# Optimization experiments

Measured on AMD Instinct MI355X. Metric: run time of the kernel, lower is better.

The kernel has to match this reference:

```python
import jax, jax.numpy as jnp
import numpy as np

B, L, S, D, H, E, UV = 4, 2048, 2048, 1024, 8, 128, 128
ROT_DIM = H * E  # RotaryEmbedding(dim=qk_size*n_heads) applied on flattened dim


def gelu(x):
    return jax.nn.gelu(x, approximate=False)  # torch nn.GELU default (erf)


def rope(x):
    # x: [B, T, ROT_DIM]; interleaved-pair rotary (lucidrains rotary_embedding_torch default)
    T = x.shape[1]
    inv_freq = 1.0 / (10000.0 ** (jnp.arange(0, ROT_DIM, 2, dtype=jnp.float32) / ROT_DIM))
    freqs = jnp.arange(T, dtype=jnp.float32)[:, None] * inv_freq  # [T, ROT_DIM/2]
    cos = jnp.repeat(jnp.cos(freqs), 2, axis=-1)  # [T, ROT_DIM]
    sin = jnp.repeat(jnp.sin(freqs), 2, axis=-1)
    xp = x.reshape(*x.shape[:-1], ROT_DIM // 2, 2)
    x_rot = jnp.stack([-xp[..., 1], xp[..., 0]], axis=-1).reshape(x.shape)
    return x * cos + x_rot * sin


def setup_inputs() -> dict:
    key = jax.random.key(0)
    ks = jax.random.split(key, 16)
    n = lambda k, sh, s=1.0: jax.random.normal(k, sh, jnp.float32) * s
    w = 0.02
    return {
        "u": n(ks[0], (B, L, D)),
        "queries": n(ks[1], (B, L, D)),
        "keys": n(ks[2], (B, S, D)),
        "values": n(ks[3], (B, S, D)),
        "Wqk": n(ks[4], (D, H * E), w), "bqk": jnp.zeros((H * E,), jnp.float32),
        "Wv": n(ks[5], (D, H * UV), w), "bv": jnp.zeros((H * UV,), jnp.float32),
        "Wu": n(ks[6], (D, H * UV), w), "bu": jnp.zeros((H * UV,), jnp.float32),
        "Wo": n(ks[7], (H * UV, D), w), "bo": jnp.zeros((D,), jnp.float32),
        "q_gamma": jnp.ones((E,), jnp.float32), "q_beta": n(ks[8], (E,), w),
        "k_gamma": jnp.ones((E,), jnp.float32), "k_beta": n(ks[9], (E,), w),
    }


def _forward(u, queries, keys, values, Wqk, bqk, Wv, bv, Wu, bu, Wo, bo,
             q_gamma, q_beta, k_gamma, k_beta):
    # use_aff=True: shared qk projection + per-branch ScaleOffset over qk_size
    qk = gelu(queries @ Wqk + bqk)                      # [B,L,H*E]
    qk4 = qk.reshape(B, L, H, E)
    q = (qk4 * q_gamma + q_beta).reshape(B, L, H * E)
    k = (qk4 * k_gamma + k_beta).reshape(B, L, H * E)
    q = rope(q).reshape(B, L, H, E)
    k = rope(k).reshape(B, S, H, E)
    v = gelu(values @ Wv + bv).reshape(B, S, H, UV)
    # Conv1d(kernel_size=1) == pointwise linear over channels
    u_p = gelu(u @ Wu + bu).reshape(B, L, H, UV)
    scale = 1.0 / jnp.sqrt(jnp.float32(E))
    scores = jnp.einsum("blhe,bshe->bhls", q, k) * scale
    attn = jax.nn.softmax(scores, axis=-1)              # [B,H,L,S]
    ctx = jnp.einsum("bhls,bshd->blhd", attn, v)        # [B,L,H,UV]
    out = (u_p * ctx).reshape(B, L, H * UV)             # gate by u
    o = out @ Wo + bo                                   # [B,L,D]
    return o, attn


def reference(u, queries, keys, values, Wqk, bqk, Wv, bv, Wu, bu, Wo, bo,
              q_gamma, q_beta, k_gamma, k_beta):
    return _forward(u, queries, keys, values, Wqk, bqk, Wv, bv, Wu, bu, Wo, bo,
                    q_gamma, q_beta, k_gamma, k_beta)
```

## Files before the change

kernel.cpp:

```cpp
#include <hip/hip_runtime.h>
#include <hip/hip_bf16.h>
#include <math.h>

#define DEVI static __device__ __forceinline__

typedef __attribute__((ext_vector_type(4))) float f32x4;
typedef __attribute__((ext_vector_type(8))) short bf16x8;
typedef __attribute__((ext_vector_type(4))) short bf16x4;

constexpr int Bc = 4, Lc = 2048, Sc = 2048, Dc = 1024, Hc = 8, Ec = 128, UVc = 128;
constexpr int HEc = Hc * Ec;
constexpr int BLc = Bc * Lc;

DEVI unsigned f2bf_bits(float f) {
  unsigned u = __builtin_bit_cast(unsigned, f);
  return (u + 0x7FFFu + ((u >> 16) & 1u)) >> 16;
}
DEVI short f2bf(float f) { return (short)f2bf_bits(f); }
DEVI float bf2f(short s) {
  return __builtin_bit_cast(float, (unsigned)((unsigned short)s) << 16);
}
DEVI float gelu_f(float x) { return 0.5f * x * (1.0f + erff(x * 0.7071067811865476f)); }

DEVI void gload16(const void* gsrc, void* ldst) {
  __builtin_amdgcn_global_load_lds(
      (const __attribute__((address_space(1))) unsigned*)gsrc,
      (__attribute__((address_space(3))) unsigned*)(ldst), 16, 0, 0);
}

DEVI f32x4 mfma16(bf16x8 a, bf16x8 b, f32x4 c) {
  return __builtin_amdgcn_mfma_f32_16x16x32_bf16(a, b, c, 0, 0, 0);
}

__global__ void cvt_bf16_kernel(const float* __restrict__ in, short* __restrict__ out) {
  size_t i = ((size_t)blockIdx.x * 256 + threadIdx.x) * 8;
  float4 f1 = *reinterpret_cast<const float4*>(in + i);
  float4 f2 = *reinterpret_cast<const float4*>(in + i + 4);
  uint4 pk;
  pk.x = f2bf_bits(f1.x) | (f2bf_bits(f1.y) << 16);
  pk.y = f2bf_bits(f1.z) | (f2bf_bits(f1.w) << 16);
  pk.z = f2bf_bits(f2.x) | (f2bf_bits(f2.y) << 16);
  pk.w = f2bf_bits(f2.z) | (f2bf_bits(f2.w) << 16);
  *reinterpret_cast<uint4*>(out + i) = pk;
}

__global__ void wt_trans_kernel(const float* __restrict__ W, short* __restrict__ WT) {
  __shared__ float t[32][33];
  int tx = threadIdx.x, ty = threadIdx.y;
  int n0 = blockIdx.x * 32, k0 = blockIdx.y * 32;
#pragma unroll
  for (int i = 0; i < 4; i++) {
    int r = ty + i * 8;
    t[r][tx] = W[(size_t)(k0 + r) * 1024 + n0 + tx];
  }
  __syncthreads();
#pragma unroll
  for (int i = 0; i < 4; i++) {
    int r = ty + i * 8;
    WT[(size_t)(n0 + r) * 1024 + k0 + tx] = f2bf(t[tx][r]);
  }
}

__global__ void rope_table_kernel(float* __restrict__ ct, float* __restrict__ st) {
  int idx = blockIdx.x * 256 + threadIdx.x;
  int t = idx >> 9, i = idx & 511;
  float inv = expf((float)i * (-9.210340371976184f / 512.0f));
  float ang = (float)t * inv;
  float sv, cv;
  sincosf(ang, &sv, &cv);
  ct[idx] = cv;
  st[idx] = sv;
}

template <bool GELU_OUT>
__global__ __launch_bounds__(256, 2) void gemm_kernel(
    const short* __restrict__ A, const short* __restrict__ BT,
    const float* __restrict__ bias, void* __restrict__ Cptr, int M, int N, int K) {
  __shared__ char smem[32768];
  const int tid = threadIdx.x;
  const int wave = tid >> 6, lane = tid & 63;
  const int lquad = lane >> 4, l15 = lane & 15;
  const int m0 = blockIdx.x * 128, n0 = blockIdx.y * 128;
  const int wr = wave >> 1, wc = wave & 1;
  f32x4 acc[4][4] = {};

  const int q0 = tid * 16, q1 = tid * 16 + 4096;
  const int r0 = q0 >> 6, o0 = (q0 & 63) ^ ((r0 & 3) << 4);
  const int r1 = q1 >> 6, o1 = (q1 & 63) ^ ((r1 & 3) << 4);
  const short* a0 = A + (size_t)(m0 + r0) * K + (o0 >> 1);
  const short* a1 = A + (size_t)(m0 + r1) * K + (o1 >> 1);
  const short* b0 = BT + (size_t)(n0 + r0) * K + (o0 >> 1);
  const short* b1 = BT + (size_t)(n0 + r1) * K + (o1 >> 1);

#define G_STAGE(buf, kt)                                   \
  {                                                        \
    char* As_ = smem + (buf)*8192;                         \
    char* Bs_ = smem + 16384 + (buf)*8192;                 \
    gload16(a0 + (kt), As_ + q0);                          \
    gload16(a1 + (kt), As_ + q1);                          \
    gload16(b0 + (kt), Bs_ + q0);                          \
    gload16(b1 + (kt), Bs_ + q1);                          \
  }

  G_STAGE(0, 0);
  asm volatile("s_waitcnt vmcnt(0)" ::: "memory");
  __builtin_amdgcn_s_barrier();

  const int NT = K >> 5;
  for (int t = 0; t < NT; t++) {
    const int cur = t & 1;
    if (t + 1 < NT) G_STAGE(cur ^ 1, (t + 1) * 32);
    __builtin_amdgcn_sched_barrier(0);
    const char* As_ = smem + cur * 8192;
    const char* Bs_ = smem + 16384 + cur * 8192;
    const int ko = lquad * 16;
    bf16x8 a[4], b[4];
#pragma unroll
    for (int f = 0; f < 4; f++) {
      int ra = wr * 64 + f * 16 + l15;
      a[f] = *reinterpret_cast<const bf16x8*>(As_ + ra * 64 + (ko ^ ((ra & 3) << 4)));
      int rb = wc * 64 + f * 16 + l15;
      b[f] = *reinterpret_cast<const bf16x8*>(Bs_ + rb * 64 + (ko ^ ((rb & 3) << 4)));
    }
#pragma unroll
    for (int mf = 0; mf < 4; mf++)
#pragma unroll
      for (int nf = 0; nf < 4; nf++)
        acc[mf][nf] = mfma16(a[mf], b[nf], acc[mf][nf]);
    asm volatile("s_waitcnt vmcnt(0) lgkmcnt(0)" ::: "memory");
    __builtin_amdgcn_sched_barrier(0);
    __builtin_amdgcn_s_barrier();
  }
#undef G_STAGE

#pragma unroll
  for (int mf = 0; mf < 4; mf++) {
#pragma unroll
    for (int nf = 0; nf < 4; nf++) {
      int mrow = m0 + wr * 64 + mf * 16 + 4 * lquad;
      int ncol = n0 + wc * 64 + nf * 16 + l15;
      float bval = bias[ncol];
#pragma unroll
      for (int r = 0; r < 4; r++) {
        float v = acc[mf][nf][r] + bval;
        if (GELU_OUT) {
          ((short*)Cptr)[(size_t)(mrow + r) * N + ncol] = f2bf(gelu_f(v));
        } else {
          ((float*)Cptr)[(size_t)(mrow + r) * N + ncol] = v;
        }
      }
    }
  }
}

__global__ void rope_apply_kernel(const short* __restrict__ qkg,
                                  const float* __restrict__ ct, const float* __restrict__ st,
                                  const float* __restrict__ qg, const float* __restrict__ qb,
                                  const float* __restrict__ kg, const float* __restrict__ kb,
                                  short* __restrict__ qo, short* __restrict__ ko) {
  int tid = blockIdx.x * 256 + threadIdx.x;
  size_t base = (size_t)tid * 8;
  int bl = (int)(base >> 10);
  int rem = (int)(base & 1023);
  int e0 = rem & 127;
  int t = bl & 2047;
  int pf = rem >> 1;
  uint4 raw = *reinterpret_cast<const uint4*>(qkg + base);
  short sh[8];
  *reinterpret_cast<uint4*>(sh) = raw;
  float4 c4 = *reinterpret_cast<const float4*>(ct + (size_t)t * 512 + pf);
  float4 s4 = *reinterpret_cast<const float4*>(st + (size_t)t * 512 + pf);
  float4 qga = *reinterpret_cast<const float4*>(qg + e0);
  float4 qgb = *reinterpret_cast<const float4*>(qg + e0 + 4);
  float4 qba = *reinterpret_cast<const float4*>(qb + e0);
  float4 qbb = *reinterpret_cast<const float4*>(qb + e0 + 4);
  float4 kga = *reinterpret_cast<const float4*>(kg + e0);
  float4 kgb = *reinterpret_cast<const float4*>(kg + e0 + 4);
  float4 kba = *reinterpret_cast<const float4*>(kb + e0);
  float4 kbb = *reinterpret_cast<const float4*>(kb + e0 + 4);
  float C[4] = {c4.x, c4.y, c4.z, c4.w};
  float Sn[4] = {s4.x, s4.y, s4.z, s4.w};
  float QG[8] = {qga.x, qga.y, qga.z, qga.w, qgb.x, qgb.y, qgb.z, qgb.w};
  float QB[8] = {qba.x, qba.y, qba.z, qba.w, qbb.x, qbb.y, qbb.z, qbb.w};
  float KG[8] = {kga.x, kga.y, kga.z, kga.w, kgb.x, kgb.y, kgb.z, kgb.w};
  float KB[8] = {kba.x, kba.y, kba.z, kba.w, kbb.x, kbb.y, kbb.z, kbb.w};
  short qsh[8], ksh[8];
#pragma unroll
  for (int j = 0; j < 4; j++) {
    float x0 = bf2f(sh[2 * j]), x1 = bf2f(sh[2 * j + 1]);
    float q0 = x0 * QG[2 * j] + QB[2 * j];
    float q1 = x1 * QG[2 * j + 1] + QB[2 * j + 1];
    qsh[2 * j] = f2bf(q0 * C[j] - q1 * Sn[j]);
    qsh[2 * j + 1] = f2bf(q1 * C[j] + q0 * Sn[j]);
    float k0v = x0 * KG[2 * j] + KB[2 * j];
    float k1v = x1 * KG[2 * j + 1] + KB[2 * j + 1];
    ksh[2 * j] = f2bf(k0v * C[j] - k1v * Sn[j]);
    ksh[2 * j + 1] = f2bf(k1v * C[j] + k0v * Sn[j]);
  }
  *reinterpret_cast<uint4*>(qo + base) = *reinterpret_cast<uint4*>(qsh);
  *reinterpret_cast<uint4*>(ko + base) = *reinterpret_cast<uint4*>(ksh);
}

__global__ void vtrans_kernel(const short* __restrict__ v, short* __restrict__ vT) {
  __shared__ short t[32][33];
  int bh = blockIdx.z;
  int b = bh >> 3, h = bh & 7;
  int s0 = blockIdx.x * 32, d0 = blockIdx.y * 32;
  int tx = threadIdx.x, ty = threadIdx.y;
#pragma unroll
  for (int i = 0; i < 4; i++) {
    int s = ty + i * 8;
    t[s][tx] = v[(((size_t)b * Sc + s0 + s) * Hc + h) * UVc + d0 + tx];
  }
  __syncthreads();
#pragma unroll
  for (int i = 0; i < 4; i++) {
    int d = ty + i * 8;
    vT[((size_t)bh * UVc + d0 + d) * Sc + s0 + tx] = t[tx][d];
  }
}

__global__ __launch_bounds__(256, 2) void attn_kernel(
    const short* __restrict__ qs, const short* __restrict__ ks,
    const short* __restrict__ vT, const short* __restrict__ up,
    float* __restrict__ attn_out, short* __restrict__ gate) {
  __shared__ char smem[65536];
  const int bid = blockIdx.x;
  const int xcd = bid & 7, jj = bid >> 3;
  const int bh = xcd * 4 + (jj >> 4);
  const int lblk = jj & 15;
  const int b = bh >> 3, h = bh & 7;
  const int l0 = lblk * 128;
  const int tid = threadIdx.x;
  const int wave = tid >> 6, lane = tid & 63;
  const int lquad = lane >> 4, l15 = lane & 15;
  const float scale = 0.08838834764831845f;

  const short* ksrc[4];
  const short* vsrc[4];
  int qdst[4];
#pragma unroll
  for (int i = 0; i < 4; i++) {
    int q = i * 4096 + tid * 16;
    qdst[i] = q;
    int row = q >> 8, off = (q & 255) ^ ((row & 7) << 4);
    ksrc[i] = ks + (((size_t)b * Sc + row) * Hc + h) * Ec + (off >> 1);
    int rv = q >> 7, ov = (q & 127) ^ ((rv & 7) << 4);
    vsrc[i] = vT + ((size_t)bh * UVc + rv) * Sc + (ov >> 1);
  }

#define STAGE_K(buf, s0)                                                     \
  {                                                                          \
    char* Kb_ = smem + (buf)*16384;                                          \
    gload16(ksrc[0] + (size_t)(s0)*1024, Kb_ + qdst[0]);                     \
    gload16(ksrc[1] + (size_t)(s0)*1024, Kb_ + qdst[1]);                     \
    gload16(ksrc[2] + (size_t)(s0)*1024, Kb_ + qdst[2]);                     \
    gload16(ksrc[3] + (size_t)(s0)*1024, Kb_ + qdst[3]);                     \
  }
#define STAGE_V(buf, s0)                                                     \
  {                                                                          \
    char* Vb_ = smem + 32768 + (buf)*16384;                                  \
    gload16(vsrc[0] + (s0), Vb_ + qdst[0]);                                  \
    gload16(vsrc[1] + (s0), Vb_ + qdst[1]);                                  \
    gload16(vsrc[2] + (s0), Vb_ + qdst[2]);                                  \
    gload16(vsrc[3] + (s0), Vb_ + qdst[3]);                                  \
  }

  bf16x8 qf[2][4];
#pragma unroll
  for (int cf = 0; cf < 2; cf++) {
    int lrow = l0 + wave * 32 + cf * 16 + l15;
    const short* qp = qs + (((size_t)b * Lc + lrow) * Hc + h) * Ec;
#pragma unroll
    for (int kt = 0; kt < 4; kt++)
      qf[cf][kt] = *reinterpret_cast<const bf16x8*>(qp + kt * 32 + lquad * 8);
  }

#define QK_TILE(KBASE, d)                                                              \
  {                                                                                    \
    const char* KB_ = (KBASE);                                                         \
    _Pragma("unroll") for (int kt = 0; kt < 4; kt++) {                                 \
      _Pragma("unroll") for (int sf = 0; sf < 4; sf++) {                               \
        int row = sf * 16 + l15;                                                       \
        bf16x8 kf = *reinterpret_cast<const bf16x8*>(                                  \
            KB_ + row * 256 + ((kt * 64 + lquad * 16) ^ ((row & 7) << 4)));            \
        d[sf][0] = mfma16(kf, qf[0][kt], d[sf][0]);                                    \
        d[sf][1] = mfma16(kf, qf[1][kt], d[sf][1]);                                    \
      }                                                                                \
    }                                                                                  \
  }

  STAGE_K(0, 0);
  asm volatile("s_waitcnt vmcnt(0)" ::: "memory");
  __builtin_amdgcn_s_barrier();
  float rs0 = 0.f, rs1 = 0.f;
  for (int t = 0; t < 32; t++) {
    const int cur = t & 1;
    if (t < 31) STAGE_K(cur ^ 1, (t + 1) * 64);
    __builtin_amdgcn_sched_barrier(0);
    f32x4 d[4][2] = {};
    QK_TILE(smem + cur * 16384, d);
#pragma unroll
    for (int sf = 0; sf < 4; sf++)
#pragma unroll
      for (int r = 0; r < 4; r++) {
        rs0 += __expf(scale * d[sf][0][r]);
        rs1 += __expf(scale * d[sf][1][r]);
      }
    asm volatile("s_waitcnt vmcnt(0) lgkmcnt(0)" ::: "memory");
    __builtin_amdgcn_sched_barrier(0);
    __builtin_amdgcn_s_barrier();
  }
  rs0 += __shfl_xor(rs0, 16);
  rs0 += __shfl_xor(rs0, 32);
  rs1 += __shfl_xor(rs1, 16);
  rs1 += __shfl_xor(rs1, 32);
  const float rcp0 = 1.0f / rs0, rcp1 = 1.0f / rs1;

  STAGE_K(0, 0);
  STAGE_V(0, 0);
  asm volatile("s_waitcnt vmcnt(0)" ::: "memory");
  __builtin_amdgcn_s_barrier();
  f32x4 ctx[8][2] = {};
  for (int t = 0; t < 32; t++) {
    const int cur = t & 1;
    const int s0 = t * 64;
    if (t < 31) {
      STAGE_K(cur ^ 1, s0 + 64);
      STAGE_V(cur ^ 1, s0 + 64);
    }
    __builtin_amdgcn_sched_barrier(0);
    f32x4 d[4][2] = {};
    QK_TILE(smem + cur * 16384, d);
#pragma unroll
    for (int sf = 0; sf < 4; sf++)
#pragma unroll
      for (int r = 0; r < 4; r++) {
        d[sf][0][r] = __expf(scale * d[sf][0][r]) * rcp0;
        d[sf][1][r] = __expf(scale * d[sf][1][r]) * rcp1;
      }
#pragma unroll
    for (int cf = 0; cf < 2; cf++) {
      int lrow = l0 + wave * 32 + cf * 16 + l15;
      float* arow = attn_out + ((size_t)bh * Lc + lrow) * Sc + s0 + lquad * 4;
#pragma unroll
      for (int sf = 0; sf < 4; sf++)
        *reinterpret_cast<f32x4*>(arow + sf * 16) = d[sf][cf];
    }
    const char* VB_ = smem + 32768 + cur * 16384;
#pragma unroll
    for (int c = 0; c < 2; c++) {
      bf16x8 pb0, pb1;
#pragma unroll
      for (int r = 0; r < 4; r++) {
        pb0[r] = f2bf(d[2 * c][0][r]);
        pb0[4 + r] = f2bf(d[2 * c + 1][0][r]);
        pb1[r] = f2bf(d[2 * c][1][r]);
        pb1[4 + r] = f2bf(d[2 * c + 1][1][r]);
      }
#pragma unroll
      for (int df = 0; df < 8; df++) {
        int dd = df * 16 + l15;
        int sw = (dd & 7) << 4;
        const char* vrow = VB_ + dd * 128;
        bf16x4 lo = *reinterpret_cast<const bf16x4*>(vrow + ((c * 64 + lquad * 8) ^ sw));
        bf16x4 hi = *reinterpret_cast<const bf16x4*>(vrow + ((c * 64 + 32 + lquad * 8) ^ sw));
        bf16x8 vf = __builtin_shufflevector(lo, hi, 0, 1, 2, 3, 4, 5, 6, 7);
        ctx[df][0] = mfma16(vf, pb0, ctx[df][0]);
        ctx[df][1] = mfma16(vf, pb1, ctx[df][1]);
      }
    }
    asm volatile("s_waitcnt vmcnt(8) lgkmcnt(0)" ::: "memory");
    __builtin_amdgcn_sched_barrier(0);
    __builtin_amdgcn_s_barrier();
  }
#undef STAGE_K
#undef STAGE_V
#undef QK_TILE

#pragma unroll
  for (int cf = 0; cf < 2; cf++) {
    int lrow = l0 + wave * 32 + cf * 16 + l15;
    size_t base = ((size_t)b * Lc + lrow) * HEc + h * UVc;
    const short* ub = up + base;
    short* gp = gate + base;
#pragma unroll
    for (int df = 0; df < 8; df++) {
      int doff = df * 16 + lquad * 4;
      bf16x4 uv = *reinterpret_cast<const bf16x4*>(ub + doff);
      bf16x4 gv;
#pragma unroll
      for (int r = 0; r < 4; r++)
        gv[r] = f2bf(bf2f(uv[r]) * ctx[df][cf][r]);
      *reinterpret_cast<bf16x4*>(gp + doff) = gv;
    }
  }
}

extern "C" void kernel_launch(void* const* d_in, const int* in_sizes, int n_in,
                              void* d_out, int out_size, void* d_ws, size_t ws_size,
                              hipStream_t stream) {
  const float* u_in = (const float*)d_in[0];
  const float* qry = (const float*)d_in[1];
  const float* vals = (const float*)d_in[3];
  const float* Wqk = (const float*)d_in[4];
  const float* bqk = (const float*)d_in[5];
  const float* Wv = (const float*)d_in[6];
  const float* bv = (const float*)d_in[7];
  const float* Wu = (const float*)d_in[8];
  const float* bu = (const float*)d_in[9];
  const float* Wo = (const float*)d_in[10];
  const float* bo = (const float*)d_in[11];
  const float* qg = (const float*)d_in[12];
  const float* qb = (const float*)d_in[13];
  const float* kg = (const float*)d_in[14];
  const float* kb = (const float*)d_in[15];

  char* w = (char*)d_ws;
  short* WT0 = (short*)w; w += (size_t)1024 * 1024 * 2;
  short* WT1 = (short*)w; w += (size_t)1024 * 1024 * 2;
  short* WT2 = (short*)w; w += (size_t)1024 * 1024 * 2;
  short* WT3 = (short*)w; w += (size_t)1024 * 1024 * 2;
  float* ctab = (float*)w; w += (size_t)2048 * 512 * 4;
  float* stab = (float*)w; w += (size_t)2048 * 512 * 4;
  const size_t BUF = (size_t)BLc * HEc * 2;
  short* C1 = (short*)w; w += BUF;
  short* C2 = (short*)w; w += BUF;
  short* C3 = (short*)w; w += BUF;
  short* qkg = (short*)w; w += BUF;
  short* qbf = (short*)w; w += BUF;
  short* kbf = (short*)w; w += BUF;
  short* vTb = (short*)w; w += BUF;
  short* upb = (short*)w; w += BUF;
  short* vgl = C1;
  short* gtb = qkg;

  float* o_out = (float*)d_out;
  float* attn_out = o_out + (size_t)BLc * Dc;

  dim3 tb(32, 8);
  cvt_bf16_kernel<<<4096, 256, 0, stream>>>(qry, C1);
  cvt_bf16_kernel<<<4096, 256, 0, stream>>>(vals, C2);
  cvt_bf16_kernel<<<4096, 256, 0, stream>>>(u_in, C3);
  wt_trans_kernel<<<dim3(32, 32), tb, 0, stream>>>(Wqk, WT0);
  wt_trans_kernel<<<dim3(32, 32), tb, 0, stream>>>(Wv, WT1);
  wt_trans_kernel<<<dim3(32, 32), tb, 0, stream>>>(Wu, WT2);
  wt_trans_kernel<<<dim3(32, 32), tb, 0, stream>>>(Wo, WT3);
  rope_table_kernel<<<4096, 256, 0, stream>>>(ctab, stab);

  gemm_kernel<true><<<dim3(64, 8), 256, 0, stream>>>(C1, WT0, bqk, qkg, BLc, HEc, Dc);
  rope_apply_kernel<<<4096, 256, 0, stream>>>(qkg, ctab, stab, qg, qb, kg, kb, qbf, kbf);
  gemm_kernel<true><<<dim3(64, 8), 256, 0, stream>>>(C2, WT1, bv, vgl, BLc, HEc, Dc);
  vtrans_kernel<<<dim3(64, 4, 32), tb, 0, stream>>>(vgl, vTb);
  gemm_kernel<true><<<dim3(64, 8), 256, 0, stream>>>(C3, WT2, bu, upb, BLc, HEc, Dc);
  attn_kernel<<<512, 256, 0, stream>>>(qbf, kbf, vTb, upb, attn_out, gtb);
  gemm_kernel<false><<<dim3(64, 8), 256, 0, stream>>>(gtb, WT3, bo, o_out, BLc, Dc, HEc);
}
```

Baseline: 422.4 us.

## Fuse fp32 conversion and rope into GEMMs, deepen K pipeline, stream attn stores

Drops the separate fp32→bf16 conversion kernels: the GEMM now loads fp32 activations into registers and converts them while writing to LDS. The rope/scale-offset step is fused into the QK GEMM epilogue, using a combined cos/sin table and a lane shuffle to fetch the pair partner. The four weight transposes are merged into one launch. The attention kernel's first pass gets a 4-deep K prefetch ring with partial vmcnt waits, and attention probability stores become nontemporal. Together these cut intermediate HBM traffic and launches, at the cost of register-path A loads in the GEMM and more scattered epilogue stores.

```diff
diff --git a/kernel.cpp b/kernel.cpp
--- a/kernel.cpp
+++ b/kernel.cpp
@@ -32,20 +32,15 @@
   return __builtin_amdgcn_mfma_f32_16x16x32_bf16(a, b, c, 0, 0, 0);
 }
 
-__global__ void cvt_bf16_kernel(const float* __restrict__ in, short* __restrict__ out) {
-  size_t i = ((size_t)blockIdx.x * 256 + threadIdx.x) * 8;
-  float4 f1 = *reinterpret_cast<const float4*>(in + i);
-  float4 f2 = *reinterpret_cast<const float4*>(in + i + 4);
-  uint4 pk;
-  pk.x = f2bf_bits(f1.x) | (f2bf_bits(f1.y) << 16);
-  pk.y = f2bf_bits(f1.z) | (f2bf_bits(f1.w) << 16);
-  pk.z = f2bf_bits(f2.x) | (f2bf_bits(f2.y) << 16);
-  pk.w = f2bf_bits(f2.z) | (f2bf_bits(f2.w) << 16);
-  *reinterpret_cast<uint4*>(out + i) = pk;
-}
-
-__global__ void wt_trans_kernel(const float* __restrict__ W, short* __restrict__ WT) {
+__global__ void wt_trans_kernel(const float* __restrict__ W0, const float* __restrict__ W1,
+                                const float* __restrict__ W2, const float* __restrict__ W3,
+                                short* __restrict__ T0, short* __restrict__ T1,
+                                short* __restrict__ T2, short* __restrict__ T3) {
   __shared__ float t[32][33];
+  const float* Ws[4] = {W0, W1, W2, W3};
+  short* Ts[4] = {T0, T1, T2, T3};
+  const float* W = Ws[blockIdx.z];
+  short* WT = Ts[blockIdx.z];
   int tx = threadIdx.x, ty = threadIdx.y;
   int n0 = blockIdx.x * 32, k0 = blockIdx.y * 32;
 #pragma unroll
@@ -61,21 +56,23 @@
   }
 }
 
-__global__ void rope_table_kernel(float* __restrict__ ct, float* __restrict__ st) {
+__global__ void rope_cs_kernel(float2* __restrict__ cs) {
   int idx = blockIdx.x * 256 + threadIdx.x;
   int t = idx >> 9, i = idx & 511;
   float inv = expf((float)i * (-9.210340371976184f / 512.0f));
-  float ang = (float)t * inv;
   float sv, cv;
-  sincosf(ang, &sv, &cv);
-  ct[idx] = cv;
-  st[idx] = sv;
-}
-
-template <bool GELU_OUT>
+  sincosf((float)t * inv, &sv, &cv);
+  cs[idx] = make_float2(cv, sv);
+}
+
+template <bool AF32, int EPI>
 __global__ __launch_bounds__(256, 2) void gemm_kernel(
-    const short* __restrict__ A, const short* __restrict__ BT,
-    const float* __restrict__ bias, void* __restrict__ Cptr, int M, int N, int K) {
+    const void* __restrict__ Aptr, const short* __restrict__ BT,
+    const float* __restrict__ bias, void* __restrict__ Cptr,
+    const float2* __restrict__ cstab,
+    const float* __restrict__ qg, const float* __restrict__ qb,
+    const float* __restrict__ kg, const float* __restrict__ kb,
+    short* __restrict__ qout, short* __restrict__ kout, int M, int N, int K) {
   __shared__ char smem[32768];
   const int tid = threadIdx.x;
   const int wave = tid >> 6, lane = tid & 63;
@@ -87,29 +84,78 @@
   const int q0 = tid * 16, q1 = tid * 16 + 4096;
   const int r0 = q0 >> 6, o0 = (q0 & 63) ^ ((r0 & 3) << 4);
   const int r1 = q1 >> 6, o1 = (q1 & 63) ^ ((r1 & 3) << 4);
-  const short* a0 = A + (size_t)(m0 + r0) * K + (o0 >> 1);
-  const short* a1 = A + (size_t)(m0 + r1) * K + (o1 >> 1);
   const short* b0 = BT + (size_t)(n0 + r0) * K + (o0 >> 1);
   const short* b1 = BT + (size_t)(n0 + r1) * K + (o1 >> 1);
-
-#define G_STAGE(buf, kt)                                   \
-  {                                                        \
-    char* As_ = smem + (buf)*8192;                         \
-    char* Bs_ = smem + 16384 + (buf)*8192;                 \
-    gload16(a0 + (kt), As_ + q0);                          \
-    gload16(a1 + (kt), As_ + q1);                          \
-    gload16(b0 + (kt), Bs_ + q0);                          \
-    gload16(b1 + (kt), Bs_ + q1);                          \
-  }
-
-  G_STAGE(0, 0);
-  asm volatile("s_waitcnt vmcnt(0)" ::: "memory");
+  const short* a0 = nullptr;
+  const short* a1 = nullptr;
+  const float* asrc = nullptr;
+  int arow = 0, ao0 = 0, ao1 = 0;
+  if (AF32) {
+    arow = tid >> 1;
+    int ahalf = tid & 1, asw = (arow & 3) << 4;
+    asrc = (const float*)Aptr + (size_t)(m0 + arow) * K + ahalf * 16;
+    ao0 = (ahalf * 32) ^ asw;
+    ao1 = (ahalf * 32 + 16) ^ asw;
+  } else {
+    a0 = (const short*)Aptr + (size_t)(m0 + r0) * K + (o0 >> 1);
+    a1 = (const short*)Aptr + (size_t)(m0 + r1) * K + (o1 >> 1);
+  }
+  float4 fa0, fa1, fa2, fa3;
+
+#define LOAD_A_F32(kt)                                \
+  {                                                   \
+    const float* s_ = asrc + (kt);                    \
+    fa0 = *reinterpret_cast<const float4*>(s_);       \
+    fa1 = *reinterpret_cast<const float4*>(s_ + 4);   \
+    fa2 = *reinterpret_cast<const float4*>(s_ + 8);   \
+    fa3 = *reinterpret_cast<const float4*>(s_ + 12);  \
+  }
+#define WRITE_A_F32(buf)                                 \
+  {                                                      \
+    char* d_ = smem + (buf)*8192 + arow * 64;            \
+    uint4 lo_, hi_;                                      \
+    lo_.x = f2bf_bits(fa0.x) | (f2bf_bits(fa0.y) << 16); \
+    lo_.y = f2bf_bits(fa0.z) | (f2bf_bits(fa0.w) << 16); \
+    lo_.z = f2bf_bits(fa1.x) | (f2bf_bits(fa1.y) << 16); \
+    lo_.w = f2bf_bits(fa1.z) | (f2bf_bits(fa1.w) << 16); \
+    hi_.x = f2bf_bits(fa2.x) | (f2bf_bits(fa2.y) << 16); \
+    hi_.y = f2bf_bits(fa2.z) | (f2bf_bits(fa2.w) << 16); \
+    hi_.z = f2bf_bits(fa3.x) | (f2bf_bits(fa3.y) << 16); \
+    hi_.w = f2bf_bits(fa3.z) | (f2bf_bits(fa3.w) << 16); \
+    *reinterpret_cast<uint4*>(d_ + ao0) = lo_;           \
+    *reinterpret_cast<uint4*>(d_ + ao1) = hi_;           \
+  }
+#define STAGE_B(buf, kt)                     \
+  {                                          \
+    char* Bs_ = smem + 16384 + (buf)*8192;   \
+    gload16(b0 + (kt), Bs_ + q0);            \
+    gload16(b1 + (kt), Bs_ + q1);            \
+  }
+#define STAGE_A_BF(buf, kt)                  \
+  {                                          \
+    char* As_ = smem + (buf)*8192;           \
+    gload16(a0 + (kt), As_ + q0);            \
+    gload16(a1 + (kt), As_ + q1);            \
+  }
+
+  if (AF32) {
+    LOAD_A_F32(0);
+    WRITE_A_F32(0);
+  } else {
+    STAGE_A_BF(0, 0);
+  }
+  STAGE_B(0, 0);
+  asm volatile("s_waitcnt vmcnt(0) lgkmcnt(0)" ::: "memory");
   __builtin_amdgcn_s_barrier();
 
   const int NT = K >> 5;
   for (int t = 0; t < NT; t++) {
     const int cur = t & 1;
-    if (t + 1 < NT) G_STAGE(cur ^ 1, (t + 1) * 32);
+    const bool pf = (t + 1 < NT);
+    if (pf) {
+      if (AF32) LOAD_A_F32((t + 1) * 32) else STAGE_A_BF(cur ^ 1, (t + 1) * 32);
+      STAGE_B(cur ^ 1, (t + 1) * 32);
+    }
     __builtin_amdgcn_sched_barrier(0);
     const char* As_ = smem + cur * 8192;
     const char* Bs_ = smem + 16384 + cur * 8192;
@@ -127,78 +173,50 @@
 #pragma unroll
       for (int nf = 0; nf < 4; nf++)
         acc[mf][nf] = mfma16(a[mf], b[nf], acc[mf][nf]);
+    if (AF32 && pf) WRITE_A_F32(cur ^ 1);
     asm volatile("s_waitcnt vmcnt(0) lgkmcnt(0)" ::: "memory");
     __builtin_amdgcn_sched_barrier(0);
     __builtin_amdgcn_s_barrier();
   }
-#undef G_STAGE
+#undef LOAD_A_F32
+#undef WRITE_A_F32
+#undef STAGE_B
+#undef STAGE_A_BF
 
 #pragma unroll
   for (int mf = 0; mf < 4; mf++) {
 #pragma unroll
     for (int nf = 0; nf < 4; nf++) {
-      int mrow = m0 + wr * 64 + mf * 16 + 4 * lquad;
-      int ncol = n0 + wc * 64 + nf * 16 + l15;
-      float bval = bias[ncol];
-#pragma unroll
-      for (int r = 0; r < 4; r++) {
-        float v = acc[mf][nf][r] + bval;
-        if (GELU_OUT) {
-          ((short*)Cptr)[(size_t)(mrow + r) * N + ncol] = f2bf(gelu_f(v));
-        } else {
-          ((float*)Cptr)[(size_t)(mrow + r) * N + ncol] = v;
+      const int mrow = m0 + wr * 64 + mf * 16 + 4 * lquad;
+      const int ncol = n0 + wc * 64 + nf * 16 + l15;
+      const float bval = bias[ncol];
+      if constexpr (EPI == 2) {
+        const int e7 = ncol & 127;
+        const float QG = qg[e7], QB = qb[e7], KG = kg[e7], KB = kb[e7];
+        const int p = ncol >> 1;
+        const float sgn = (ncol & 1) ? 1.0f : -1.0f;
+#pragma unroll
+        for (int r = 0; r < 4; r++) {
+          const int m = mrow + r;
+          const int tt = m & 2047;
+          float2 cs = cstab[(size_t)tt * 512 + p];
+          float g = gelu_f(acc[mf][nf][r] + bval);
+          float qv = g * QG + QB, kv = g * KG + KB;
+          float pq = __shfl_xor(qv, 1), pk = __shfl_xor(kv, 1);
+          qout[(size_t)m * N + ncol] = f2bf(qv * cs.x + sgn * pq * cs.y);
+          kout[(size_t)m * N + ncol] = f2bf(kv * cs.x + sgn * pk * cs.y);
         }
+      } else if constexpr (EPI == 1) {
+#pragma unroll
+        for (int r = 0; r < 4; r++)
+          ((short*)Cptr)[(size_t)(mrow + r) * N + ncol] = f2bf(gelu_f(acc[mf][nf][r] + bval));
+      } else {
+#pragma unroll
+        for (int r = 0; r < 4; r++)
+          ((float*)Cptr)[(size_t)(mrow + r) * N + ncol] = acc[mf][nf][r] + bval;
       }
     }
   }
-}
-
-__global__ void rope_apply_kernel(const short* __restrict__ qkg,
-                                  const float* __restrict__ ct, const float* __restrict__ st,
-                                  const float* __restrict__ qg, const float* __restrict__ qb,
-                                  const float* __restrict__ kg, const float* __restrict__ kb,
-                                  short* __restrict__ qo, short* __restrict__ ko) {
-  int tid = blockIdx.x * 256 + threadIdx.x;
-  size_t base = (size_t)tid * 8;
-  int bl = (int)(base >> 10);
-  int rem = (int)(base & 1023);
-  int e0 = rem & 127;
-  int t = bl & 2047;
-  int pf = rem >> 1;
-  uint4 raw = *reinterpret_cast<const uint4*>(qkg + base);
-  short sh[8];
-  *reinterpret_cast<uint4*>(sh) = raw;
-  float4 c4 = *reinterpret_cast<const float4*>(ct + (size_t)t * 512 + pf);
-  float4 s4 = *reinterpret_cast<const float4*>(st + (size_t)t * 512 + pf);
-  float4 qga = *reinterpret_cast<const float4*>(qg + e0);
-  float4 qgb = *reinterpret_cast<const float4*>(qg + e0 + 4);
-  float4 qba = *reinterpret_cast<const float4*>(qb + e0);
-  float4 qbb = *reinterpret_cast<const float4*>(qb + e0 + 4);
-  float4 kga = *reinterpret_cast<const float4*>(kg + e0);
-  float4 kgb = *reinterpret_cast<const float4*>(kg + e0 + 4);
-  float4 kba = *reinterpret_cast<const float4*>(kb + e0);
-  float4 kbb = *reinterpret_cast<const float4*>(kb + e0 + 4);
-  float C[4] = {c4.x, c4.y, c4.z, c4.w};
-  float Sn[4] = {s4.x, s4.y, s4.z, s4.w};
-  float QG[8] = {qga.x, qga.y, qga.z, qga.w, qgb.x, qgb.y, qgb.z, qgb.w};
-  float QB[8] = {qba.x, qba.y, qba.z, qba.w, qbb.x, qbb.y, qbb.z, qbb.w};
-  float KG[8] = {kga.x, kga.y, kga.z, kga.w, kgb.x, kgb.y, kgb.z, kgb.w};
-  float KB[8] = {kba.x, kba.y, kba.z, kba.w, kbb.x, kbb.y, kbb.z, kbb.w};
-  short qsh[8], ksh[8];
-#pragma unroll
-  for (int j = 0; j < 4; j++) {
-    float x0 = bf2f(sh[2 * j]), x1 = bf2f(sh[2 * j + 1]);
-    float q0 = x0 * QG[2 * j] + QB[2 * j];
-    float q1 = x1 * QG[2 * j + 1] + QB[2 * j + 1];
-    qsh[2 * j] = f2bf(q0 * C[j] - q1 * Sn[j]);
-    qsh[2 * j + 1] = f2bf(q1 * C[j] + q0 * Sn[j]);
-    float k0v = x0 * KG[2 * j] + KB[2 * j];
-    float k1v = x1 * KG[2 * j + 1] + KB[2 * j + 1];
-    ksh[2 * j] = f2bf(k0v * C[j] - k1v * Sn[j]);
-    ksh[2 * j + 1] = f2bf(k1v * C[j] + k0v * Sn[j]);
-  }
-  *reinterpret_cast<uint4*>(qo + base) = *reinterpret_cast<uint4*>(qsh);
-  *reinterpret_cast<uint4*>(ko + base) = *reinterpret_cast<uint4*>(ksh);
 }
 
 __global__ void vtrans_kernel(const short* __restrict__ v, short* __restrict__ vT) {
@@ -249,21 +267,21 @@
     vsrc[i] = vT + ((size_t)bh * UVc + rv) * Sc + (ov >> 1);
   }
 
-#define STAGE_K(buf, s0)                                                     \
-  {                                                                          \
-    char* Kb_ = smem + (buf)*16384;                                          \
-    gload16(ksrc[0] + (size_t)(s0)*1024, Kb_ + qdst[0]);                     \
-    gload16(ksrc[1] + (size_t)(s0)*1024, Kb_ + qdst[1]);                     \
-    gload16(ksrc[2] + (size_t)(s0)*1024, Kb_ + qdst[2]);                     \
-    gload16(ksrc[3] + (size_t)(s0)*1024, Kb_ + qdst[3]);                     \
-  }
-#define STAGE_V(buf, s0)                                                     \
-  {                                                                          \
-    char* Vb_ = smem + 32768 + (buf)*16384;                                  \
-    gload16(vsrc[0] + (s0), Vb_ + qdst[0]);                                  \
-    gload16(vsrc[1] + (s0), Vb_ + qdst[1]);                                  \
-    gload16(vsrc[2] + (s0), Vb_ + qdst[2]);                                  \
-    gload16(vsrc[3] + (s0), Vb_ + qdst[3]);                                  \
+#define STAGE_K(buf, s0)                                  \
+  {                                                       \
+    char* Kb_ = smem + (buf)*16384;                       \
+    gload16(ksrc[0] + (size_t)(s0)*1024, Kb_ + qdst[0]);  \
+    gload16(ksrc[1] + (size_t)(s0)*1024, Kb_ + qdst[1]);  \
+    gload16(ksrc[2] + (size_t)(s0)*1024, Kb_ + qdst[2]);  \
+    gload16(ksrc[3] + (size_t)(s0)*1024, Kb_ + qdst[3]);  \
+  }
+#define STAGE_V(buf, s0)                     \
+  {                                          \
+    char* Vb_ = smem + 32768 + (buf)*16384;  \
+    gload16(vsrc[0] + (s0), Vb_ + qdst[0]);  \
+    gload16(vsrc[1] + (s0), Vb_ + qdst[1]);  \
+    gload16(vsrc[2] + (s0), Vb_ + qdst[2]);  \
+    gload16(vsrc[3] + (s0), Vb_ + qdst[3]);  \
   }
 
   bf16x8 qf[2][4];
@@ -275,31 +293,40 @@
     for (int kt = 0; kt < 4; kt++)
       qf[cf][kt] = *reinterpret_cast<const bf16x8*>(qp + kt * 32 + lquad * 8);
   }
-
-#define QK_TILE(KBASE, d)                                                              \
-  {                                                                                    \
-    const char* KB_ = (KBASE);                                                         \
-    _Pragma("unroll") for (int kt = 0; kt < 4; kt++) {                                 \
-      _Pragma("unroll") for (int sf = 0; sf < 4; sf++) {                               \
-        int row = sf * 16 + l15;                                                       \
-        bf16x8 kf = *reinterpret_cast<const bf16x8*>(                                  \
-            KB_ + row * 256 + ((kt * 64 + lquad * 16) ^ ((row & 7) << 4)));            \
-        d[sf][0] = mfma16(kf, qf[0][kt], d[sf][0]);                                    \
-        d[sf][1] = mfma16(kf, qf[1][kt], d[sf][1]);                                    \
-      }                                                                                \
-    }                                                                                  \
+  __builtin_amdgcn_sched_barrier(0);
+
+#define QK_TILE(KBASE, d)                                                   \
+  {                                                                         \
+    const char* KB_ = (KBASE);                                              \
+    _Pragma("unroll") for (int kt = 0; kt < 4; kt++) {                      \
+      _Pragma("unroll") for (int sf = 0; sf < 4; sf++) {                    \
+        int row = sf * 16 + l15;                                            \
+        bf16x8 kf = *reinterpret_cast<const bf16x8*>(                       \
+            KB_ + row * 256 + ((kt * 64 + lquad * 16) ^ ((row & 7) << 4))); \
+        d[sf][0] = mfma16(kf, qf[0][kt], d[sf][0]);                         \
+        d[sf][1] = mfma16(kf, qf[1][kt], d[sf][1]);                         \
+      }                                                                     \
+    }                                                                       \
   }
 
   STAGE_K(0, 0);
-  asm volatile("s_waitcnt vmcnt(0)" ::: "memory");
-  __builtin_amdgcn_s_barrier();
+  __builtin_amdgcn_sched_barrier(0);
+  STAGE_K(1, 64);
+  __builtin_amdgcn_sched_barrier(0);
+  STAGE_K(2, 128);
+  __builtin_amdgcn_sched_barrier(0);
   float rs0 = 0.f, rs1 = 0.f;
   for (int t = 0; t < 32; t++) {
-    const int cur = t & 1;
-    if (t < 31) STAGE_K(cur ^ 1, (t + 1) * 64);
-    __builtin_amdgcn_sched_barrier(0);
+    if (t < 30)
+      asm volatile("s_waitcnt vmcnt(8)" ::: "memory");
+    else if (t == 30)
+      asm volatile("s_waitcnt vmcnt(4)" ::: "memory");
+    else
+      asm volatile("s_waitcnt vmcnt(0)" ::: "memory");
+    __builtin_amdgcn_sched_barrier(0);
+    __builtin_amdgcn_s_barrier();
     f32x4 d[4][2] = {};
-    QK_TILE(smem + cur * 16384, d);
+    QK_TILE(smem + (t & 3) * 16384, d);
 #pragma unroll
     for (int sf = 0; sf < 4; sf++)
 #pragma unroll
@@ -307,9 +334,10 @@
         rs0 += __expf(scale * d[sf][0][r]);
         rs1 += __expf(scale * d[sf][1][r]);
       }
-    asm volatile("s_waitcnt vmcnt(0) lgkmcnt(0)" ::: "memory");
+    asm volatile("s_waitcnt lgkmcnt(0)" ::: "memory");
     __builtin_amdgcn_sched_barrier(0);
     __builtin_amdgcn_s_barrier();
+    if (t < 29) STAGE_K((t + 3) & 3, (t + 3) * 64);
   }
   rs0 += __shfl_xor(rs0, 16);
   rs0 += __shfl_xor(rs0, 32);
@@ -345,7 +373,7 @@
       float* arow = attn_out + ((size_t)bh * Lc + lrow) * Sc + s0 + lquad * 4;
 #pragma unroll
       for (int sf = 0; sf < 4; sf++)
-        *reinterpret_cast<f32x4*>(arow + sf * 16) = d[sf][cf];
+        __builtin_nontemporal_store(d[sf][cf], reinterpret_cast<f32x4*>(arow + sf * 16));
     }
     const char* VB_ = smem + 32768 + cur * 16384;
 #pragma unroll
@@ -421,38 +449,33 @@
   short* WT1 = (short*)w; w += (size_t)1024 * 1024 * 2;
   short* WT2 = (short*)w; w += (size_t)1024 * 1024 * 2;
   short* WT3 = (short*)w; w += (size_t)1024 * 1024 * 2;
-  float* ctab = (float*)w; w += (size_t)2048 * 512 * 4;
-  float* stab = (float*)w; w += (size_t)2048 * 512 * 4;
+  float2* cstab = (float2*)w; w += (size_t)2048 * 512 * 8;
   const size_t BUF = (size_t)BLc * HEc * 2;
-  short* C1 = (short*)w; w += BUF;
-  short* C2 = (short*)w; w += BUF;
-  short* C3 = (short*)w; w += BUF;
-  short* qkg = (short*)w; w += BUF;
   short* qbf = (short*)w; w += BUF;
   short* kbf = (short*)w; w += BUF;
+  short* vgl = (short*)w; w += BUF;
   short* vTb = (short*)w; w += BUF;
   short* upb = (short*)w; w += BUF;
-  short* vgl = C1;
-  short* gtb = qkg;
+  short* gtb = (short*)w; w += BUF;
 
   float* o_out = (float*)d_out;
   float* attn_out = o_out + (size_t)BLc * Dc;
 
   dim3 tb(32, 8);
-  cvt_bf16_kernel<<<4096, 256, 0, stream>>>(qry, C1);
-  cvt_bf16_kernel<<<4096, 256, 0, stream>>>(vals, C2);
-  cvt_bf16_kernel<<<4096, 256, 0, stream>>>(u_in, C3);
-  wt_trans_kernel<<<dim3(32, 32), tb, 0, stream>>>(Wqk, WT0);
-  wt_trans_kernel<<<dim3(32, 32), tb, 0, stream>>>(Wv, WT1);
-  wt_trans_kernel<<<dim3(32, 32), tb, 0, stream>>>(Wu, WT2);
-  wt_trans_kernel<<<dim3(32, 32), tb, 0, stream>>>(Wo, WT3);
-  rope_table_kernel<<<4096, 256, 0, stream>>>(ctab, stab);
-
-  gemm_kernel<true><<<dim3(64, 8), 256, 0, stream>>>(C1, WT0, bqk, qkg, BLc, HEc, Dc);
-  rope_apply_kernel<<<4096, 256, 0, stream>>>(qkg, ctab, stab, qg, qb, kg, kb, qbf, kbf);
-  gemm_kernel<true><<<dim3(64, 8), 256, 0, stream>>>(C2, WT1, bv, vgl, BLc, HEc, Dc);
+  wt_trans_kernel<<<dim3(32, 32, 4), tb, 0, stream>>>(Wqk, Wv, Wu, Wo, WT0, WT1, WT2, WT3);
+  rope_cs_kernel<<<4096, 256, 0, stream>>>(cstab);
+
+  gemm_kernel<true, 2><<<dim3(64, 8), 256, 0, stream>>>(
+      qry, WT0, bqk, nullptr, cstab, qg, qb, kg, kb, qbf, kbf, BLc, HEc, Dc);
+  gemm_kernel<true, 1><<<dim3(64, 8), 256, 0, stream>>>(
+      vals, WT1, bv, vgl, nullptr, nullptr, nullptr, nullptr, nullptr, nullptr, nullptr,
+      BLc, HEc, Dc);
   vtrans_kernel<<<dim3(64, 4, 32), tb, 0, stream>>>(vgl, vTb);
-  gemm_kernel<true><<<dim3(64, 8), 256, 0, stream>>>(C3, WT2, bu, upb, BLc, HEc, Dc);
+  gemm_kernel<true, 1><<<dim3(64, 8), 256, 0, stream>>>(
+      u_in, WT2, bu, upb, nullptr, nullptr, nullptr, nullptr, nullptr, nullptr, nullptr,
+      BLc, HEc, Dc);
   attn_kernel<<<512, 256, 0, stream>>>(qbf, kbf, vTb, upb, attn_out, gtb);
-  gemm_kernel<false><<<dim3(64, 8), 256, 0, stream>>>(gtb, WT3, bo, o_out, BLc, Dc, HEc);
-}
+  gemm_kernel<false, 0><<<dim3(64, 8), 256, 0, stream>>>(
+      gtb, WT3, bo, o_out, nullptr, nullptr, nullptr, nullptr, nullptr, nullptr, nullptr,
+      BLc, Dc, HEc);
+}
```

New measurement: 437.8 us. 1.04x slower.
